# Performance work log

Hardware: AMD Instinct MI355X
Metric: run time of the kernel (lower is better)

Reference implementation:

```python
import jax, jax.numpy as jnp
import numpy as np

EPS = 1e-3  # matches torch module eps
NUM_FEATURES = 64


def setup_inputs() -> dict:
    key = jax.random.key(0)
    X = jax.random.normal(key, (128, NUM_FEATURES, 56, 56), dtype=jnp.float32)
    return {"X": X}


def reference(X):
    # Training-mode decorrelated batch norm (ZCA whitening via eigendecomposition).
    N, C = X.shape[0], X.shape[1]
    # [N, C, H, W] -> [C, N*H*W]
    x = jnp.reshape(jnp.swapaxes(X, 0, 1), (C, -1))
    m = x.shape[1]
    mean = jnp.mean(x, axis=-1, keepdims=True)
    xc = x - mean
    # sigma = eps*I + (1/m) * xc @ xc^T   (C x C, SPD)
    sigma = EPS * jnp.eye(C, dtype=X.dtype) + (xc @ xc.T) / m
    # SVD of an SPD matrix == eigendecomposition; use symmetric eigh.
    eig, u = jnp.linalg.eigh(sigma)
    # wm = u @ diag(eig^-1/2) @ u^T  (inverse matrix square root)
    wm = (u * jax.lax.rsqrt(eig)) @ u.T
    xn = wm @ xc  # whiten
    # [C, N*H*W] -> [N, C, H, W]
    Xn = jnp.swapaxes(jnp.reshape(xn, (C, N) + X.shape[2:]), 0, 1)
    return Xn
```

## Files before the change

kernel.cpp:

```cpp
#include <hip/hip_runtime.h>
#include <stdint.h>

#define CCH   64
#define HWSZ  3136
#define NB    128
#define MCOLS 401408
#define TK    128
#define NTILES 3136
#define LDK   136
#define LDB   72
#define SLOT  4160
#define WS_TAIL 12416
#define RG    32
#define K1MAX 1024

typedef short bf16x8 __attribute__((ext_vector_type(8)));
typedef float f32x4  __attribute__((ext_vector_type(4)));

__device__ __forceinline__ unsigned short f2bf(float f) {
    union { float f; uint32_t u; } v; v.f = f;
    uint32_t r = v.u + 0x7fffu + ((v.u >> 16) & 1u);
    return (unsigned short)(r >> 16);
}
__device__ __forceinline__ float bf2f(unsigned short h) {
    union { uint32_t u; float f; } v; v.u = ((uint32_t)h) << 16; return v.f;
}

__global__ __launch_bounds__(256) void k1_gram(const float* __restrict__ X,
                                               float* __restrict__ part,
                                               int nb) {
    __shared__ __align__(16) unsigned short tile[CCH * LDK];
    const int tid = threadIdx.x;
    const int w = tid >> 6, l = tid & 63;

    f32x4 acc[4];
    #pragma unroll
    for (int b = 0; b < 4; ++b) acc[b] = (f32x4){0.f, 0.f, 0.f, 0.f};
    float sacc[16];
    #pragma unroll
    for (int i = 0; i < 16; ++i) sacc[i] = 0.f;

    float2 xv[16];

    uint32_t t = blockIdx.x;
    {
        const uint32_t s = t * TK + 2u * (uint32_t)l;
        const uint32_t n = s / HWSZ;
        const uint32_t hw = s - n * HWSZ;
        const size_t base = (size_t)n * (CCH * HWSZ) + hw + (size_t)w * HWSZ;
        #pragma unroll
        for (int i = 0; i < 16; ++i)
            xv[i] = *(const float2*)(X + base + (size_t)i * (4u * HWSZ));
    }

    for (;;) {
        __syncthreads();
        #pragma unroll
        for (int i = 0; i < 16; ++i) {
            sacc[i] += xv[i].x + xv[i].y;
            const int c = 4 * i + w;
            *(uint32_t*)&tile[c * LDK + 2 * l] =
                (uint32_t)f2bf(xv[i].x) | ((uint32_t)f2bf(xv[i].y) << 16);
        }
        __syncthreads();

        const uint32_t tn = t + (uint32_t)nb;
        const bool more = tn < NTILES;
        if (more) {
            const uint32_t s = tn * TK + 2u * (uint32_t)l;
            const uint32_t n = s / HWSZ;
            const uint32_t hw = s - n * HWSZ;
            const size_t base = (size_t)n * (CCH * HWSZ) + hw + (size_t)w * HWSZ;
            #pragma unroll
            for (int i = 0; i < 16; ++i)
                xv[i] = *(const float2*)(X + base + (size_t)i * (4u * HWSZ));
        }

        #pragma unroll
        for (int k0 = 0; k0 < TK; k0 += 32) {
            const int koff = k0 + ((l >> 4) << 3);
            const bf16x8 fa = *(const bf16x8*)&tile[(16 * w + (l & 15)) * LDK + koff];
            #pragma unroll
            for (int bj = 0; bj < 4; ++bj) {
                const bf16x8 fb = *(const bf16x8*)&tile[(16 * bj + (l & 15)) * LDK + koff];
                acc[bj] = __builtin_amdgcn_mfma_f32_16x16x32_bf16(fa, fb, acc[bj], 0, 0, 0);
            }
        }

        if (!more) break;
        t = tn;
    }

    float* pg = part + (size_t)blockIdx.x * SLOT;
    #pragma unroll
    for (int bj = 0; bj < 4; ++bj) {
        #pragma unroll
        for (int r = 0; r < 4; ++r) {
            const int row = 16 * w + ((l >> 4) << 2) + r;
            const int col = 16 * bj + (l & 15);
            pg[row * 64 + col] = acc[bj][r];
        }
    }
    #pragma unroll
    for (int i = 0; i < 16; ++i) {
        float v = sacc[i];
        #pragma unroll
        for (int m = 32; m > 0; m >>= 1) v += __shfl_xor(v, m, 64);
        if (l == 0) pg[4096 + 4 * i + w] = v;
    }
}

__global__ __launch_bounds__(256) void k1b1_reduce(const float* __restrict__ part,
                                                   float* __restrict__ part2,
                                                   int nb) {
    const int bx = blockIdx.x;
    const int g = bx / 17;
    const int e = (bx - g * 17) * 256 + threadIdx.x;
    if (e >= SLOT) return;
    float a0 = 0.f, a1 = 0.f, a2 = 0.f, a3 = 0.f;
    int b = g;
    for (; b + 3 * RG < nb; b += 4 * RG) {
        a0 += part[(size_t)b * SLOT + e];
        a1 += part[(size_t)(b + RG) * SLOT + e];
        a2 += part[(size_t)(b + 2 * RG) * SLOT + e];
        a3 += part[(size_t)(b + 3 * RG) * SLOT + e];
    }
    for (; b < nb; b += RG) a0 += part[(size_t)b * SLOT + e];
    part2[(size_t)g * SLOT + e] = (a0 + a1) + (a2 + a3);
}

__global__ __launch_bounds__(256) void k1b2_reduce(const float* __restrict__ part2,
                                                   float* __restrict__ out) {
    const int e = blockIdx.x * 256 + threadIdx.x;
    if (e >= SLOT) return;
    float a0 = 0.f, a1 = 0.f, a2 = 0.f, a3 = 0.f;
    #pragma unroll
    for (int b = 0; b < RG; b += 4) {
        a0 += part2[(size_t)b * SLOT + e];
        a1 += part2[(size_t)(b + 1) * SLOT + e];
        a2 += part2[(size_t)(b + 2) * SLOT + e];
        a3 += part2[(size_t)(b + 3) * SLOT + e];
    }
    out[e] = (a0 + a1) + (a2 + a3);
}

__device__ __forceinline__ bf16x8 ldfrag_h(const unsigned short* H, int rowbase, int k0, int l) {
    const int row = rowbase + (l & 15);
    const int koff = k0 + ((l >> 4) << 3);
    return *(const bf16x8*)&H[row * LDB + koff];
}
__device__ __forceinline__ bf16x8 ldfrag_lo(const float* F, bf16x8 hi, int rowbase, int k0, int l) {
    const int row = rowbase + (l & 15);
    const int koff = k0 + ((l >> 4) << 3);
    const float* p = F + row * 64 + koff;
    bf16x8 lo;
    #pragma unroll
    for (int j = 0; j < 8; ++j)
        lo[j] = (short)f2bf(p[j] - bf2f((unsigned short)hi[j]));
    return lo;
}

__device__ void mm_plain(const unsigned short* Lh, const unsigned short* Rh,
                         unsigned short* DH, float* DF, int tid) {
    const int w = tid >> 6, l = tid & 63;
    f32x4 acc[4];
    #pragma unroll
    for (int b = 0; b < 4; ++b) acc[b] = (f32x4){0.f, 0.f, 0.f, 0.f};
    #pragma unroll
    for (int k0 = 0; k0 < 64; k0 += 32) {
        const bf16x8 la = ldfrag_h(Lh, 16 * w, k0, l);
        #pragma unroll
        for (int b = 0; b < 4; ++b) {
            const bf16x8 rb = ldfrag_h(Rh, 16 * b, k0, l);
            acc[b] = __builtin_amdgcn_mfma_f32_16x16x32_bf16(la, rb, acc[b], 0, 0, 0);
        }
    }
    __syncthreads();
    #pragma unroll
    for (int b = 0; b < 4; ++b) {
        #pragma unroll
        for (int r = 0; r < 4; ++r) {
            const int row = 16 * w + ((l >> 4) << 2) + r;
            const int col = 16 * b + (l & 15);
            const float v = acc[b][r];
            if (DH) DH[row * LDB + col] = f2bf(v);
            if (DF) DF[row * 64 + col] = v;
        }
    }
    __syncthreads();
}

__device__ void mm_split(const unsigned short* Lh, const float* Lf,
                         const unsigned short* Rh, const float* Rf,
                         unsigned short* DH, float* DF, int tid) {
    const int w = tid >> 6, l = tid & 63;
    f32x4 acc[4];
    #pragma unroll
    for (int b = 0; b < 4; ++b) acc[b] = (f32x4){0.f, 0.f, 0.f, 0.f};
    #pragma unroll
    for (int k0 = 0; k0 < 64; k0 += 32) {
        const bf16x8 lah = ldfrag_h(Lh, 16 * w, k0, l);
        const bf16x8 lal = ldfrag_lo(Lf, lah, 16 * w, k0, l);
        #pragma unroll
        for (int b = 0; b < 4; ++b) {
            const bf16x8 rbh = ldfrag_h(Rh, 16 * b, k0, l);
            const bf16x8 rbl = ldfrag_lo(Rf, rbh, 16 * b, k0, l);
            acc[b] = __builtin_amdgcn_mfma_f32_16x16x32_bf16(lah, rbh, acc[b], 0, 0, 0);
            acc[b] = __builtin_amdgcn_mfma_f32_16x16x32_bf16(lah, rbl, acc[b], 0, 0, 0);
            acc[b] = __builtin_amdgcn_mfma_f32_16x16x32_bf16(lal, rbh, acc[b], 0, 0, 0);
        }
    }
    __syncthreads();
    #pragma unroll
    for (int b = 0; b < 4; ++b) {
        #pragma unroll
        for (int r = 0; r < 4; ++r) {
            const int row = 16 * w + ((l >> 4) << 2) + r;
            const int col = 16 * b + (l & 15);
            const float v = acc[b][r];
            if (DH) DH[row * LDB + col] = f2bf(v);
            if (DF) DF[row * 64 + col] = v;
        }
    }
    __syncthreads();
}

__global__ __launch_bounds__(256) void k2_ns(float* __restrict__ ws) {
    const float* gram = ws;
    const float* sums = ws + 4096;
    float* wm = ws + 4160;
    float* bvec = ws + 8256;
    float* Ag = ws + 8320;

    __shared__ float Zf[4096];
    __shared__ float Sf[4096];
    __shared__ __align__(16) unsigned short Ah[64 * LDB];
    __shared__ __align__(16) unsigned short ZhA[64 * LDB];
    __shared__ __align__(16) unsigned short Bh[64 * LDB];
    __shared__ float mu[64];
    __shared__ float sred[1];

    const int tid = threadIdx.x;
    const float invm = 1.0f / (float)MCOLS;

    if (tid < 64) mu[tid] = sums[tid] * invm;
    __syncthreads();

    #pragma unroll
    for (int j = 0; j < 16; ++j) {
        const int e = tid * 16 + j;
        const int i = e >> 6, c = e & 63;
        Sf[e] = gram[e] * invm - mu[i] * mu[c] + ((i == c) ? 1e-3f : 0.0f);
    }
    __syncthreads();

    if (tid < 64) {
        float rs = 0.f;
        #pragma unroll
        for (int j = 0; j < 64; ++j) {
            const int c = (j + tid) & 63;
            rs += fabsf(Sf[tid * 64 + c]);
        }
        #pragma unroll
        for (int m = 32; m > 0; m >>= 1) rs = fmaxf(rs, __shfl_xor(rs, m, 64));
        if (tid == 0) sred[0] = rs;
    }
    __syncthreads();
    const float s = sred[0];
    const float invs = 1.0f / s;

    #pragma unroll
    for (int j = 0; j < 16; ++j) {
        const int e = tid * 16 + j;
        const int i = e >> 6, c = e & 63;
        const float a = Sf[e] * invs;
        Ag[e] = a;
        Ah[i * LDB + c] = f2bf(a);
        const float z = (i == c) ? 1.0f : 0.0f;
        Zf[e] = z;
        ZhA[i * LDB + c] = f2bf(z);
    }
    __syncthreads();

    for (int itn = 0; itn < 4; ++itn) {
        mm_plain(ZhA, ZhA, Bh, nullptr, tid);
        mm_plain(Ah, Bh, Bh, nullptr, tid);
        mm_plain(ZhA, Bh, nullptr, Sf, tid);
        #pragma unroll
        for (int j = 0; j < 16; ++j) {
            const int e = tid * 16 + j;
            const int i = e >> 6, c = e & 63;
            const float z = 1.5f * Zf[e] - 0.5f * Sf[e];
            Zf[e] = z;
            ZhA[i * LDB + c] = f2bf(z);
        }
        __syncthreads();
    }

    mm_split(ZhA, Zf, ZhA, Zf, Bh, Sf, tid);
    mm_split(Ah, Ag, Bh, Sf, Bh, Sf, tid);
    mm_split(ZhA, Zf, Bh, Sf, nullptr, Sf, tid);

    const float wsq = 1.0f / sqrtf(s);
    #pragma unroll
    for (int j = 0; j < 16; ++j) {
        const int e = tid * 16 + j;
        const float z = 1.5f * Zf[e] - 0.5f * Sf[e];
        Zf[e] = z;
        wm[e] = z * wsq;
    }
    __syncthreads();

    if (tid < 64) {
        float acc = 0.f;
        #pragma unroll
        for (int j = 0; j < 64; ++j) {
            const int c = (j + tid) & 63;
            acc += Zf[tid * 64 + c] * mu[c];
        }
        bvec[tid] = acc * wsq;
    }
}

__global__ __launch_bounds__(256) void k3_whiten(const float* __restrict__ X,
                                                 const float* __restrict__ wm,
                                                 const float* __restrict__ bvec,
                                                 float* __restrict__ out) {
    __shared__ float xs[64 * 64];
    const int tid = threadIdx.x;
    const int l = tid & 63;
    const int wq = __builtin_amdgcn_readfirstlane(tid >> 6) * 16;

    const uint32_t g = blockIdx.x;
    const uint32_t n = g / 49u;
    const uint32_t hw0 = (g - n * 49u) * 64u;
    const size_t base = (size_t)n * (CCH * HWSZ) + hw0;

    #pragma unroll
    for (int cb = 0; cb < 4; ++cb) {
        const int cp = cb * 16 + (tid >> 4);
        const int p4 = (tid & 15) * 4;
        *(f32x4*)&xs[cp * 64 + p4] =
            *(const f32x4*)(X + base + (size_t)cp * HWSZ + p4);
    }
    __syncthreads();

    float acc[16];
    #pragma unroll
    for (int j = 0; j < 16; ++j) acc[j] = 0.f;

    #pragma unroll 2
    for (int cp = 0; cp < 64; ++cp) {
        const float xv = xs[cp * 64 + l];
        const float* wr = wm + cp * 64 + wq;
        #pragma unroll
        for (int j = 0; j < 16; ++j) acc[j] = fmaf(wr[j], xv, acc[j]);
    }

    #pragma unroll
    for (int j = 0; j < 16; ++j)
        out[base + (size_t)(wq + j) * HWSZ + l] = acc[j] - bvec[wq + j];
}

extern "C" void kernel_launch(void* const* d_in, const int* in_sizes, int n_in,
                              void* d_out, int out_size, void* d_ws, size_t ws_size,
                              hipStream_t stream) {
    (void)in_sizes; (void)n_in; (void)out_size;
    const float* X = (const float*)d_in[0];
    float* out = (float*)d_out;
    float* ws = (float*)d_ws;

    long avail = (long)(ws_size / sizeof(float)) - WS_TAIL - (long)RG * SLOT;
    int nb = (int)(avail / SLOT);
    if (nb > K1MAX) nb = K1MAX;
    if (nb < 1) nb = 1;

    float* part = ws + WS_TAIL;
    float* part2 = part + (size_t)nb * SLOT;

    k1_gram<<<nb, 256, 0, stream>>>(X, part, nb);
    k1b1_reduce<<<17 * RG, 256, 0, stream>>>(part, part2, nb);
    k1b2_reduce<<<17, 256, 0, stream>>>(part2, ws);
    k2_ns<<<1, 256, 0, stream>>>(ws);
    k3_whiten<<<MCOLS / 64, 256, 0, stream>>>(X, ws + 4160, ws + 8256, out);
}
```

Measured before the change: 250.1 us.

## Use split-bf16 MFMA for whitening matmul with transposed LDS tile

The whitening kernel now performs the 64x64 by 64-column matmul with bf16 MFMA instructions instead of scalar FP32 FMAs. Both the whitening matrix and the input tile are split into high and low bf16 parts, and three MFMAs per tile approximate FP32 accuracy. k2 now writes the whitening matrix as two bf16 arrays in a new workspace region, and output stores become 16-byte vector writes. This cuts ALU work in a kernel that streams about 100 MB each way, at the cost of conversion work, some precision loss, and a larger workspace tail.

```diff
diff --git a/kernel.cpp b/kernel.cpp
--- a/kernel.cpp
+++ b/kernel.cpp
@@ -10,12 +10,14 @@
 #define LDK   136
 #define LDB   72
 #define SLOT  4160
-#define WS_TAIL 12416
+#define WS_TAIL 16512
 #define RG    32
 #define K1MAX 1024
+#define LDT   72
 
 typedef short bf16x8 __attribute__((ext_vector_type(8)));
 typedef float f32x4  __attribute__((ext_vector_type(4)));
+typedef unsigned short u16x4 __attribute__((ext_vector_type(4)));
 
 __device__ __forceinline__ unsigned short f2bf(float f) {
     union { float f; uint32_t u; } v; v.f = f;
@@ -228,9 +230,10 @@
 __global__ __launch_bounds__(256) void k2_ns(float* __restrict__ ws) {
     const float* gram = ws;
     const float* sums = ws + 4096;
-    float* wm = ws + 4160;
     float* bvec = ws + 8256;
     float* Ag = ws + 8320;
+    unsigned short* wmh = (unsigned short*)(ws + 12416);
+    unsigned short* wml = (unsigned short*)(ws + 14464);
 
     __shared__ float Zf[4096];
     __shared__ float Sf[4096];
@@ -307,7 +310,10 @@
         const int e = tid * 16 + j;
         const float z = 1.5f * Zf[e] - 0.5f * Sf[e];
         Zf[e] = z;
-        wm[e] = z * wsq;
+        const float wv = z * wsq;
+        const unsigned short h = f2bf(wv);
+        wmh[e] = h;
+        wml[e] = f2bf(wv - bf2f(h));
     }
     __syncthreads();
 
@@ -322,14 +328,17 @@
     }
 }
 
-__global__ __launch_bounds__(256) void k3_whiten(const float* __restrict__ X,
-                                                 const float* __restrict__ wm,
-                                                 const float* __restrict__ bvec,
-                                                 float* __restrict__ out) {
-    __shared__ float xs[64 * 64];
+__global__ __launch_bounds__(256, 2) void k3_whiten(const float* __restrict__ X,
+                                                    const float* __restrict__ ws,
+                                                    float* __restrict__ out) {
+    __shared__ __align__(16) unsigned short xh[64 * LDT];
+    __shared__ __align__(16) unsigned short xl[64 * LDT];
     const int tid = threadIdx.x;
-    const int l = tid & 63;
-    const int wq = __builtin_amdgcn_readfirstlane(tid >> 6) * 16;
+    const int w = tid >> 6, l = tid & 63;
+
+    const unsigned short* __restrict__ wmh = (const unsigned short*)(ws + 12416);
+    const unsigned short* __restrict__ wml = (const unsigned short*)(ws + 14464);
+    const float* __restrict__ bvec = ws + 8256;
 
     const uint32_t g = blockIdx.x;
     const uint32_t n = g / 49u;
@@ -337,29 +346,55 @@
     const size_t base = (size_t)n * (CCH * HWSZ) + hw0;
 
     #pragma unroll
+    for (int u = 0; u < 4; ++u) {
+        const int c0 = (w * 4 + u) * 4;
+        float x0 = X[base + (size_t)(c0 + 0) * HWSZ + l];
+        float x1 = X[base + (size_t)(c0 + 1) * HWSZ + l];
+        float x2 = X[base + (size_t)(c0 + 2) * HWSZ + l];
+        float x3 = X[base + (size_t)(c0 + 3) * HWSZ + l];
+        u16x4 hv, lv;
+        hv[0] = f2bf(x0); lv[0] = f2bf(x0 - bf2f(hv[0]));
+        hv[1] = f2bf(x1); lv[1] = f2bf(x1 - bf2f(hv[1]));
+        hv[2] = f2bf(x2); lv[2] = f2bf(x2 - bf2f(hv[2]));
+        hv[3] = f2bf(x3); lv[3] = f2bf(x3 - bf2f(hv[3]));
+        *(u16x4*)&xh[l * LDT + c0] = hv;
+        *(u16x4*)&xl[l * LDT + c0] = lv;
+    }
+    __syncthreads();
+
+    f32x4 acc[4];
+    #pragma unroll
+    for (int b = 0; b < 4; ++b) acc[b] = (f32x4){0.f, 0.f, 0.f, 0.f};
+
+    const int frow = (16 * w + (l & 15)) * LDT;
+    const int koffL = (l >> 4) << 3;
+    #pragma unroll
+    for (int k0 = 0; k0 < 64; k0 += 32) {
+        const bf16x8 fah = *(const bf16x8*)&xh[frow + k0 + koffL];
+        const bf16x8 fal = *(const bf16x8*)&xl[frow + k0 + koffL];
+        #pragma unroll
+        for (int cb = 0; cb < 4; ++cb) {
+            const int c = cb * 16 + (l & 15);
+            const bf16x8 fbh = *(const bf16x8*)&wmh[c * 64 + k0 + koffL];
+            const bf16x8 fbl = *(const bf16x8*)&wml[c * 64 + k0 + koffL];
+            acc[cb] = __builtin_amdgcn_mfma_f32_16x16x32_bf16(fah, fbh, acc[cb], 0, 0, 0);
+            acc[cb] = __builtin_amdgcn_mfma_f32_16x16x32_bf16(fah, fbl, acc[cb], 0, 0, 0);
+            acc[cb] = __builtin_amdgcn_mfma_f32_16x16x32_bf16(fal, fbh, acc[cb], 0, 0, 0);
+        }
+    }
+
+    const int p0 = 16 * w + ((l >> 4) << 2);
+    #pragma unroll
     for (int cb = 0; cb < 4; ++cb) {
-        const int cp = cb * 16 + (tid >> 4);
-        const int p4 = (tid & 15) * 4;
-        *(f32x4*)&xs[cp * 64 + p4] =
-            *(const f32x4*)(X + base + (size_t)cp * HWSZ + p4);
-    }
-    __syncthreads();
-
-    float acc[16];
-    #pragma unroll
-    for (int j = 0; j < 16; ++j) acc[j] = 0.f;
-
-    #pragma unroll 2
-    for (int cp = 0; cp < 64; ++cp) {
-        const float xv = xs[cp * 64 + l];
-        const float* wr = wm + cp * 64 + wq;
-        #pragma unroll
-        for (int j = 0; j < 16; ++j) acc[j] = fmaf(wr[j], xv, acc[j]);
-    }
-
-    #pragma unroll
-    for (int j = 0; j < 16; ++j)
-        out[base + (size_t)(wq + j) * HWSZ + l] = acc[j] - bvec[wq + j];
+        const int c = cb * 16 + (l & 15);
+        const float bv = bvec[c];
+        f32x4 v;
+        v[0] = acc[cb][0] - bv;
+        v[1] = acc[cb][1] - bv;
+        v[2] = acc[cb][2] - bv;
+        v[3] = acc[cb][3] - bv;
+        *(f32x4*)&out[base + (size_t)c * HWSZ + p0] = v;
+    }
 }
 
 extern "C" void kernel_launch(void* const* d_in, const int* in_sizes, int n_in,
@@ -382,5 +417,5 @@
     k1b1_reduce<<<17 * RG, 256, 0, stream>>>(part, part2, nb);
     k1b2_reduce<<<17, 256, 0, stream>>>(part2, ws);
     k2_ns<<<1, 256, 0, stream>>>(ws);
-    k3_whiten<<<MCOLS / 64, 256, 0, stream>>>(X, ws + 4160, ws + 8256, out);
-}
+    k3_whiten<<<MCOLS / 64, 256, 0, stream>>>(X, ws, out);
+}
```

After: 269.5 us. 1.08x slower.
